# Kernel optimization log

Hardware: AMD Instinct MI355X
Metric: run time of the kernel (lower is better)

The kernel has to match this reference:

```python
import jax, jax.numpy as jnp
import numpy as np

B, IN_E, IN_I, D = 4096, 4096, 4096, 2048
IN_BR = 8192
BS = IN_BR // D  # block size = 4
K_E, K_I = 50, 1
E_TO_I = 50.0
BN_EPS = 1e-5


def setup_inputs() -> dict:
    key = jax.random.key(0)
    ks = jax.random.split(key, 8)
    # fan-in uniform init like nn.Linear (kaiming-uniform bound ~ 1/sqrt(in))
    def linw(k, out_f, in_f):
        b = 1.0 / np.sqrt(in_f)
        return jax.random.uniform(k, (out_f, in_f), jnp.float32, -b, b)
    return {
        "excitatory_input": jax.random.normal(ks[0], (B, IN_E), jnp.float32),
        "inhibitory_input": jax.random.normal(ks[1], (B, IN_I), jnp.float32),
        "dendrite_branch_outputs": jax.random.uniform(ks[2], (B, IN_BR), jnp.float32),
        "w_exc": linw(ks[3], D, IN_E),
        "w_inh": linw(ks[4], D, IN_I),
        "w_block": linw(ks[5], D, IN_BR),
        "bn_gamma": jnp.ones((D,), jnp.float32),
        "bn_beta": jnp.zeros((D,), jnp.float32),
    }


def _topk_linear(x, w, k):
    # keep the k largest weights per output row, zero the rest, then matmul
    idx = jax.lax.top_k(w, k)[1]                          # [D, k]
    mask = jnp.zeros_like(w).at[jnp.arange(w.shape[0])[:, None], idx].set(1.0)
    return x @ (w * mask).T                               # [B, D]


def _block_linear(x, w):
    # block-diagonal mask: row c uses columns [c*BS, (c+1)*BS)
    out_f = w.shape[0]
    wb = w.reshape(out_f, out_f, BS)[jnp.arange(out_f), jnp.arange(out_f)]  # [D, BS]
    xb = x.reshape(x.shape[0], out_f, BS)                                   # [B, D, BS]
    return jnp.einsum('bds,ds->bd', xb, wb)


def reference(excitatory_input, inhibitory_input, dendrite_branch_outputs,
              w_exc, w_inh, w_block, bn_gamma, bn_beta):
    dendrite_excitation = _topk_linear(excitatory_input, w_exc, K_E)
    dendrite_inhibition = _topk_linear(inhibitory_input, w_inh, K_I)
    dendrite_depolarization = _block_linear(dendrite_branch_outputs, w_block)
    total_excitatory = dendrite_excitation + dendrite_depolarization
    # neuron_type == 'excitatory'
    act = total_excitatory - E_TO_I * dendrite_inhibition
    # BatchNorm1d, training mode: batch stats, biased variance
    mean = jnp.mean(act, axis=0)
    var = jnp.var(act, axis=0)
    act = (act - mean) * jax.lax.rsqrt(var + BN_EPS) * bn_gamma + bn_beta
    return jax.nn.sigmoid(act)
```

## Files before the change

### kernel.cpp

```cpp
#include <hip/hip_runtime.h>
#include <hip/hip_fp16.h>

#define B_     4096
#define INE_   4096
#define INBR_  8192
#define D_     2048
#define KE_    50
#define KPAD_  52
#define CAP_   512

__device__ __forceinline__ unsigned packh2(float a, float b) {
  __half2 h = __floats2half2_rn(a, b);
  return __builtin_bit_cast(unsigned, h);
}
__device__ __forceinline__ float2 unpackh2(unsigned u) {
  __half2 h = __builtin_bit_cast(__half2, u);
  return __half22float2(h);
}

__device__ void topk_body(const float* __restrict__ W, int row, int k, int kpad,
                          float hi, float t0, float vscale,
                          uint4* __restrict__ muT,
                          unsigned* __restrict__ out_off, float* __restrict__ out_val)
{
  const int t = threadIdx.x;
  const float* wr = W + (size_t)row * INE_;

  __shared__ float cval[CAP_];
  __shared__ int   ccol[CAP_];
  __shared__ int   scnt;
  __shared__ int   red[4];

  float thr = t0;
  int M = 0;
  for (int attempt = 0; attempt < 8; ++attempt) {
    int local = 0;
    #pragma unroll
    for (int j = 0; j < 4; ++j) {
      float4 w4 = *reinterpret_cast<const float4*>(wr + 4 * (t + 256 * j));
      local += (w4.x > thr) + (w4.y > thr) + (w4.z > thr) + (w4.w > thr);
    }
    #pragma unroll
    for (int off = 32; off > 0; off >>= 1) local += __shfl_down(local, off);
    if ((t & 63) == 0) red[t >> 6] = local;
    __syncthreads();
    M = red[0] + red[1] + red[2] + red[3];
    __syncthreads();
    if (M >= k && M <= CAP_) break;
    if (M < k) thr = hi - (hi - thr) * 4.0f;
    else       thr = hi - (hi - thr) * 0.5f;
  }

  if (t == 0) scnt = 0;
  __syncthreads();
  #pragma unroll
  for (int j = 0; j < 4; ++j) {
    int cbase = 4 * (t + 256 * j);
    float4 w4 = *reinterpret_cast<const float4*>(wr + cbase);
    float wv[4] = {w4.x, w4.y, w4.z, w4.w};
    #pragma unroll
    for (int q = 0; q < 4; ++q) {
      if (wv[q] > thr) {
        int pp = atomicAdd(&scnt, 1);
        if (pp < CAP_) { cval[pp] = wv[q]; ccol[pp] = cbase + q; }
      }
    }
  }
  __syncthreads();
  M = scnt < CAP_ ? scnt : CAP_;

  for (int i = t; i < M; i += 256) {
    float wi = cval[i]; int ci = ccol[i];
    int rank = 0;
    for (int m = 0; m < M; ++m) {
      float wm = cval[m]; int cm = ccol[m];
      rank += (wm > wi || (wm == wi && cm < ci)) ? 1 : 0;
    }
    if (rank < k) {
      unsigned c = (unsigned)ci;
      unsigned off = ((c >> 2) << 3) | ((c & 3u) << 13);
      if (kpad == 1) {
        out_off[row] = off;
        out_val[row] = wi * vscale;
      } else {
        char* rec = (char*)muT + ((size_t)(rank >> 2) * D_ + row) * 16;
        reinterpret_cast<unsigned short*>(rec)[rank & 3] = (unsigned short)off;
        reinterpret_cast<__half*>(rec)[4 + (rank & 3)] =
            __float2half_rn(wi * vscale);
      }
    }
  }
  if (kpad > 1 && t < kpad - k) {
    int slot = k + t;
    char* rec = (char*)muT + ((size_t)(slot >> 2) * D_ + row) * 16;
    reinterpret_cast<unsigned short*>(rec)[slot & 3] = 0;
    reinterpret_cast<__half*>(rec)[4 + (slot & 3)] = __float2half_rn(0.0f);
  }
}

__global__ __launch_bounds__(256) void prep_kernel(
    const float* __restrict__ wexc, const float* __restrict__ winh,
    const float* __restrict__ wblk,
    uint4* __restrict__ muT,
    unsigned* __restrict__ so_inh, float* __restrict__ vi_inh,
    float* __restrict__ wdiag)
{
  const int bid = blockIdx.x;
  const float hi = 0.015625f;
  if (bid < 2048) {
    topk_body(wexc, bid, KE_, KPAD_, hi, hi * (1.0f - 200.0f / 4096.0f), 1.0f,
              muT, nullptr, nullptr);
  } else if (bid < 4096) {
    topk_body(winh, bid - 2048, 1, 1, hi, hi * (1.0f - 48.0f / 4096.0f), -50.0f,
              nullptr, so_inh, vi_inh);
  } else {
    const int t = threadIdx.x;
    #pragma unroll
    for (int j = 0; j < 8; ++j) {
      int d = t + 256 * j;
      float4 w = *reinterpret_cast<const float4*>(wblk + (size_t)d * (INBR_ + 4));
      reinterpret_cast<float4*>(wdiag)[d] = w;
    }
  }
}

__device__ __forceinline__ uint2 ld8(const char* ldsb, unsigned off) {
  return *reinterpret_cast<const uint2*>(ldsb + off);
}

#define FMA4(R, G, WV) do {                                                \
    float2 f0 = unpackh2((G).x), f1 = unpackh2((G).y);                     \
    acc[R][0] = fmaf(f0.x, (WV), acc[R][0]);                               \
    acc[R][1] = fmaf(f0.y, (WV), acc[R][1]);                               \
    acc[R][2] = fmaf(f1.x, (WV), acc[R][2]);                               \
    acc[R][3] = fmaf(f1.y, (WV), acc[R][3]);                               \
  } while (0)

__device__ __forceinline__ void do_br(float (&acc)[4][4], int t, int b0,
                                      const float* __restrict__ xbr,
                                      const float* __restrict__ wdiag) {
  #pragma unroll
  for (int r = 0; r < 4; ++r) {
    const int d = t + 512 * r;
    float4 wb4 = reinterpret_cast<const float4*>(wdiag)[d];
    #pragma unroll
    for (int b = 0; b < 4; ++b) {
      float4 xb4 = *reinterpret_cast<const float4*>(
          xbr + (size_t)(b0 + b) * INBR_ + 4 * d);
      acc[r][b] += xb4.x * wb4.x + xb4.y * wb4.y + xb4.z * wb4.z + xb4.w * wb4.w;
    }
  }
}

__global__ __launch_bounds__(512, 8) void fused_ei(
    const float* __restrict__ xe, const float* __restrict__ xi,
    const float* __restrict__ xbr, const float* __restrict__ wdiag,
    const uint4* __restrict__ muT,
    const unsigned* __restrict__ so_inh, const float* __restrict__ vi_inh,
    float* __restrict__ act)
{
  __shared__ unsigned xs[8192];
  const int t  = threadIdx.x;
  const int b0 = blockIdx.x * 4;
  const int p  = t & 1;
  const int Q  = t >> 1;

  float acc[4][4];
  #pragma unroll
  for (int r = 0; r < 4; ++r)
    #pragma unroll
    for (int b = 0; b < 4; ++b) acc[r][b] = 0.0f;

  const char* ldsb = reinterpret_cast<const char*>(xs);
  const bool brf = (blockIdx.x & 1);

  if (brf) do_br(acc, t, b0, xbr, wdiag);

  {
    const float* r0p = xe + (size_t)(b0 + 2 * p)     * INE_;
    const float* r1p = xe + (size_t)(b0 + 2 * p + 1) * INE_;
    #pragma unroll
    for (int m = 0; m < 4; ++m) {
      int c0 = 4 * Q + 1024 * m;
      float4 fa = *reinterpret_cast<const float4*>(r0p + c0);
      float4 fb = *reinterpret_cast<const float4*>(r1p + c0);
      int wb = 2 * (Q + 256 * m) + p;
      xs[wb]        = packh2(fa.x, fb.x);
      xs[wb + 2048] = packh2(fa.y, fb.y);
      xs[wb + 4096] = packh2(fa.z, fb.z);
      xs[wb + 6144] = packh2(fa.w, fb.w);
    }
  }

  float4 xia[4];
  {
    const float* xr0 = xi + (size_t)(b0 + 2 * p) * INE_;
    #pragma unroll
    for (int m = 0; m < 4; ++m)
      xia[m] = *reinterpret_cast<const float4*>(xr0 + 4 * Q + 1024 * m);
  }
  unsigned oi[4]; float viv[4];
  #pragma unroll
  for (int r = 0; r < 4; ++r) {
    oi[r]  = so_inh[t + 512 * r];
    viv[r] = vi_inh[t + 512 * r];
  }
  __syncthreads();

  for (int ii = 0; ii < KPAD_ / 4; ++ii) {
    uint4 m[4];
    #pragma unroll
    for (int r = 0; r < 4; ++r) m[r] = muT[ii * D_ + t + 512 * r];
    #pragma unroll
    for (int half = 0; half < 2; ++half) {
      uint2 g[2][4];
      #pragma unroll
      for (int rr = 0; rr < 2; ++rr) {
        const int r = 2 * half + rr;
        g[rr][0] = ld8(ldsb, m[r].x & 0xFFFFu);
        g[rr][1] = ld8(ldsb, m[r].x >> 16);
        g[rr][2] = ld8(ldsb, m[r].y & 0xFFFFu);
        g[rr][3] = ld8(ldsb, m[r].y >> 16);
      }
      #pragma unroll
      for (int rr = 0; rr < 2; ++rr) {
        const int r = 2 * half + rr;
        float2 vA = unpackh2(m[r].z);
        float2 vB = unpackh2(m[r].w);
        FMA4(r, g[rr][0], vA.x);
        FMA4(r, g[rr][1], vA.y);
        FMA4(r, g[rr][2], vB.x);
        FMA4(r, g[rr][3], vB.y);
      }
    }
  }
  __syncthreads();

  {
    const float* xr1 = xi + (size_t)(b0 + 2 * p + 1) * INE_;
    #pragma unroll
    for (int m = 0; m < 4; ++m) {
      int c0 = 4 * Q + 1024 * m;
      float4 fb = *reinterpret_cast<const float4*>(xr1 + c0);
      int wb = 2 * (Q + 256 * m) + p;
      xs[wb]        = packh2(xia[m].x, fb.x);
      xs[wb + 2048] = packh2(xia[m].y, fb.y);
      xs[wb + 4096] = packh2(xia[m].z, fb.z);
      xs[wb + 6144] = packh2(xia[m].w, fb.w);
    }
  }
  __syncthreads();

  {
    uint2 gi[4];
    #pragma unroll
    for (int r = 0; r < 4; ++r) gi[r] = ld8(ldsb, oi[r]);
    #pragma unroll
    for (int r = 0; r < 4; ++r) FMA4(r, gi[r], viv[r]);
  }

  if (!brf) do_br(acc, t, b0, xbr, wdiag);

  #pragma unroll
  for (int r = 0; r < 4; ++r) {
    const int d = t + 512 * r;
    #pragma unroll
    for (int b = 0; b < 4; ++b)
      act[(size_t)(b0 + b) * D_ + d] = acc[r][b];
  }
}

__global__ __launch_bounds__(256) void reduce_stats(
    const float* __restrict__ act, float* __restrict__ sums,
    float* __restrict__ sumsq)
{
  const int dg = blockIdx.x & 63;
  const int rg = blockIdx.x >> 6;
  const int tx = threadIdx.x & 31;
  const int ty = threadIdx.x >> 5;
  const int d  = dg * 32 + tx;

  float s = 0.0f, s2 = 0.0f;
  #pragma unroll 4
  for (int i = 0; i < 64; ++i) {
    int row = rg * 512 + ty + 8 * i;
    float a = act[(size_t)row * D_ + d];
    s += a;
    s2 = fmaf(a, a, s2);
  }
  __shared__ float ls[2][8][32];
  ls[0][ty][tx] = s;
  ls[1][ty][tx] = s2;
  __syncthreads();
  if (ty == 0) {
    #pragma unroll
    for (int j = 1; j < 8; ++j) { s += ls[0][j][tx]; s2 += ls[1][j][tx]; }
    atomicAdd(&sums[d], s);
    atomicAdd(&sumsq[d], s2);
  }
}

__global__ __launch_bounds__(256) void tail_kernel(
    const float* __restrict__ act, float* __restrict__ out,
    const float* __restrict__ sums, const float* __restrict__ sumsq,
    const float* __restrict__ gamma, const float* __restrict__ beta)
{
  __shared__ float scsh[2 * D_];
  const int tid = threadIdx.x;
  #pragma unroll
  for (int j = 0; j < 8; ++j) {
    int d = tid + 256 * j;
    float mean = sums[d]  * (1.0f / B_);
    float var  = sumsq[d] * (1.0f / B_) - mean * mean;
    float rstd = rsqrtf(var + 1e-5f);
    float sc   = gamma[d] * rstd;
    scsh[2 * d]     = sc;
    scsh[2 * d + 1] = fmaf(-mean, sc, beta[d]);
  }
  __syncthreads();

  const int r0 = blockIdx.x * 8;
  for (int rr = 0; rr < 8; ++rr) {
    const float4* ap = reinterpret_cast<const float4*>(act + (size_t)(r0 + rr) * D_);
    float4*       op = reinterpret_cast<float4*>(out + (size_t)(r0 + rr) * D_);
    #pragma unroll
    for (int i2 = 0; i2 < 2; ++i2) {
      int i = tid + 256 * i2;
      float4 a = ap[i];
      const float4* sp = reinterpret_cast<const float4*>(scsh + 8 * i);
      float4 s0 = sp[0];
      float4 s1 = sp[1];
      float z0 = fmaf(a.x, s0.x, s0.y);
      float z1 = fmaf(a.y, s0.z, s0.w);
      float z2 = fmaf(a.z, s1.x, s1.y);
      float z3 = fmaf(a.w, s1.z, s1.w);
      float4 o;
      o.x = 1.0f / (1.0f + __expf(-z0));
      o.y = 1.0f / (1.0f + __expf(-z1));
      o.z = 1.0f / (1.0f + __expf(-z2));
      o.w = 1.0f / (1.0f + __expf(-z3));
      op[i] = o;
    }
  }
}

extern "C" void kernel_launch(void* const* d_in, const int* in_sizes, int n_in,
                              void* d_out, int out_size, void* d_ws, size_t ws_size,
                              hipStream_t stream) {
  const float* xe    = (const float*)d_in[0];
  const float* xi    = (const float*)d_in[1];
  const float* xbr   = (const float*)d_in[2];
  const float* wexc  = (const float*)d_in[3];
  const float* winh  = (const float*)d_in[4];
  const float* wblk  = (const float*)d_in[5];
  const float* gamma = (const float*)d_in[6];
  const float* beta  = (const float*)d_in[7];
  float* out = (float*)d_out;

  char* ws = (char*)d_ws;
  uint4*    muT    = (uint4*)   (ws + 0);
  unsigned* so_inh = (unsigned*)(ws + 425984);
  float*    vi_inh = (float*)   (ws + 434176);
  float*    wdiag  = (float*)   (ws + 442368);
  float*    sums   = (float*)   (ws + 475136);
  float*    sumsq  = (float*)   (ws + 483328);
  float*    act    = (float*)   (ws + 1048576);

  hipMemsetAsync(sums, 0, 2 * D_ * sizeof(float), stream);

  prep_kernel<<<dim3(4097), dim3(256), 0, stream>>>(
      wexc, winh, wblk, muT, so_inh, vi_inh, wdiag);
  fused_ei<<<dim3(B_ / 4), dim3(512), 0, stream>>>(
      xe, xi, xbr, wdiag, muT, so_inh, vi_inh, act);
  reduce_stats<<<dim3(512), dim3(256), 0, stream>>>(act, sums, sumsq);
  tail_kernel<<<dim3(512), dim3(256), 0, stream>>>(
      act, out, sums, sumsq, gamma, beta);
}
```

Measured before the change: 144.8 us.

## Fuse batch-norm statistics accumulation into main kernel with sliced atomics

Removes the separate reduce_stats kernel by having fused_ei accumulate per-column sum and sum of squares from its register results via atomics into 4 partial slices. The tail kernel combines the slices. This avoids rereading the full activation buffer and one kernel launch, at the cost of many more global atomic operations. Launch bounds are also relaxed from 8 to 4 blocks per CU, which may change register allocation and occupancy.

```diff
diff --git a/kernel.cpp b/kernel.cpp
--- a/kernel.cpp
+++ b/kernel.cpp
@@ -8,6 +8,7 @@
 #define KE_    50
 #define KPAD_  52
 #define CAP_   512
+#define NSL_   4
 
 __device__ __forceinline__ unsigned packh2(float a, float b) {
   __half2 h = __floats2half2_rn(a, b);
@@ -152,12 +153,13 @@
   }
 }
 
-__global__ __launch_bounds__(512, 8) void fused_ei(
+__global__ __launch_bounds__(512, 4) void fused_ei(
     const float* __restrict__ xe, const float* __restrict__ xi,
     const float* __restrict__ xbr, const float* __restrict__ wdiag,
     const uint4* __restrict__ muT,
     const unsigned* __restrict__ so_inh, const float* __restrict__ vi_inh,
-    float* __restrict__ act)
+    float* __restrict__ act, float* __restrict__ sums_p,
+    float* __restrict__ sumsq_p)
 {
   __shared__ unsigned xs[8192];
   const int t  = threadIdx.x;
@@ -261,48 +263,26 @@
 
   if (!brf) do_br(acc, t, b0, xbr, wdiag);
 
+  const int slice = blockIdx.x & (NSL_ - 1);
   #pragma unroll
   for (int r = 0; r < 4; ++r) {
     const int d = t + 512 * r;
-    #pragma unroll
-    for (int b = 0; b < 4; ++b)
-      act[(size_t)(b0 + b) * D_ + d] = acc[r][b];
-  }
-}
-
-__global__ __launch_bounds__(256) void reduce_stats(
-    const float* __restrict__ act, float* __restrict__ sums,
-    float* __restrict__ sumsq)
-{
-  const int dg = blockIdx.x & 63;
-  const int rg = blockIdx.x >> 6;
-  const int tx = threadIdx.x & 31;
-  const int ty = threadIdx.x >> 5;
-  const int d  = dg * 32 + tx;
-
-  float s = 0.0f, s2 = 0.0f;
-  #pragma unroll 4
-  for (int i = 0; i < 64; ++i) {
-    int row = rg * 512 + ty + 8 * i;
-    float a = act[(size_t)row * D_ + d];
-    s += a;
-    s2 = fmaf(a, a, s2);
-  }
-  __shared__ float ls[2][8][32];
-  ls[0][ty][tx] = s;
-  ls[1][ty][tx] = s2;
-  __syncthreads();
-  if (ty == 0) {
-    #pragma unroll
-    for (int j = 1; j < 8; ++j) { s += ls[0][j][tx]; s2 += ls[1][j][tx]; }
-    atomicAdd(&sums[d], s);
-    atomicAdd(&sumsq[d], s2);
+    float s = 0.0f, s2 = 0.0f;
+    #pragma unroll
+    for (int b = 0; b < 4; ++b) {
+      float a = acc[r][b];
+      act[(size_t)(b0 + b) * D_ + d] = a;
+      s += a;
+      s2 = fmaf(a, a, s2);
+    }
+    atomicAdd(&sums_p[slice * D_ + d], s);
+    atomicAdd(&sumsq_p[slice * D_ + d], s2);
   }
 }
 
 __global__ __launch_bounds__(256) void tail_kernel(
     const float* __restrict__ act, float* __restrict__ out,
-    const float* __restrict__ sums, const float* __restrict__ sumsq,
+    const float* __restrict__ sums_p, const float* __restrict__ sumsq_p,
     const float* __restrict__ gamma, const float* __restrict__ beta)
 {
   __shared__ float scsh[2 * D_];
@@ -310,8 +290,14 @@
   #pragma unroll
   for (int j = 0; j < 8; ++j) {
     int d = tid + 256 * j;
-    float mean = sums[d]  * (1.0f / B_);
-    float var  = sumsq[d] * (1.0f / B_) - mean * mean;
+    float s = 0.0f, s2 = 0.0f;
+    #pragma unroll
+    for (int sl = 0; sl < NSL_; ++sl) {
+      s  += sums_p[sl * D_ + d];
+      s2 += sumsq_p[sl * D_ + d];
+    }
+    float mean = s  * (1.0f / B_);
+    float var  = s2 * (1.0f / B_) - mean * mean;
     float rstd = rsqrtf(var + 1e-5f);
     float sc   = gamma[d] * rstd;
     scsh[2 * d]     = sc;
@@ -358,21 +344,20 @@
   float* out = (float*)d_out;
 
   char* ws = (char*)d_ws;
-  uint4*    muT    = (uint4*)   (ws + 0);
-  unsigned* so_inh = (unsigned*)(ws + 425984);
-  float*    vi_inh = (float*)   (ws + 434176);
-  float*    wdiag  = (float*)   (ws + 442368);
-  float*    sums   = (float*)   (ws + 475136);
-  float*    sumsq  = (float*)   (ws + 483328);
-  float*    act    = (float*)   (ws + 1048576);
-
-  hipMemsetAsync(sums, 0, 2 * D_ * sizeof(float), stream);
+  uint4*    muT     = (uint4*)   (ws + 0);
+  unsigned* so_inh  = (unsigned*)(ws + 425984);
+  float*    vi_inh  = (float*)   (ws + 434176);
+  float*    wdiag   = (float*)   (ws + 442368);
+  float*    sums_p  = (float*)   (ws + 475136);
+  float*    sumsq_p = (float*)   (ws + 507904);
+  float*    act     = (float*)   (ws + 1048576);
+
+  hipMemsetAsync(sums_p, 0, 2 * NSL_ * D_ * sizeof(float), stream);
 
   prep_kernel<<<dim3(4097), dim3(256), 0, stream>>>(
       wexc, winh, wblk, muT, so_inh, vi_inh, wdiag);
   fused_ei<<<dim3(B_ / 4), dim3(512), 0, stream>>>(
-      xe, xi, xbr, wdiag, muT, so_inh, vi_inh, act);
-  reduce_stats<<<dim3(512), dim3(256), 0, stream>>>(act, sums, sumsq);
+      xe, xi, xbr, wdiag, muT, so_inh, vi_inh, act, sums_p, sumsq_p);
   tail_kernel<<<dim3(512), dim3(256), 0, stream>>>(
-      act, out, sums, sumsq, gamma, beta);
-}
+      act, out, sums_p, sumsq_p, gamma, beta);
+}
```

New measurement: 125.8 us. 13.1% less time.
